# Kernel tuning notes

Measured on AMD Instinct MI355X. Metric: run time of the kernel, lower is better.

The kernel has to match this reference:

```python
import jax, jax.numpy as jnp
import numpy as np

N = 100000
E = 1600000
D_IN, D_HID, D_OUT = 128, 128, 128


def gcn_conv(x, edge_index, W, b):
    """PyG GCNConv with default symmetric normalization and added self-loops.
    out = D^{-1/2} (A + I) D^{-1/2} (x W) + b, edge weights = 1.
    """
    n = x.shape[0]
    h = x @ W                                   # [N, D_out]
    src, dst = edge_index[0], edge_index[1]     # messages flow src -> dst
    ones = jnp.ones(src.shape[0], dtype=x.dtype)
    # degree includes the self-loop (+1), computed on the target index as in PyG
    deg = jax.ops.segment_sum(ones, dst, num_segments=n) + 1.0  # [N]
    dinv = jax.lax.rsqrt(deg)                   # deg >= 1 so safe
    norm = dinv[src] * dinv[dst]                # [E]
    msg = h[src] * norm[:, None]                # [E, D_out]
    agg = jax.ops.segment_sum(msg, dst, num_segments=n)
    # self-loop contribution: norm = dinv_i * dinv_i = 1/deg_i
    out = agg + h * (dinv * dinv)[:, None] + b
    return out


def layer_norm(x, gamma, beta, eps=1e-5):
    mu = jnp.mean(x, axis=-1, keepdims=True)
    var = jnp.mean(jnp.square(x - mu), axis=-1, keepdims=True)
    return (x - mu) * jax.lax.rsqrt(var + eps) * gamma + beta


def setup_inputs() -> dict:
    key = jax.random.key(0)
    ks = jax.random.split(key, 8)
    x = jax.random.normal(ks[0], (N, D_IN), dtype=jnp.float32)
    edge_index = jax.random.randint(ks[1], (2, E), 0, N, dtype=jnp.int64)
    s1 = 1.0 / np.sqrt(D_IN)
    s2 = 1.0 / np.sqrt(D_HID)
    W1 = jax.random.uniform(ks[2], (D_IN, D_HID), jnp.float32, -s1, s1)
    b1 = jnp.zeros((D_HID,), jnp.float32)
    W2 = jax.random.uniform(ks[3], (D_HID, D_OUT), jnp.float32, -s2, s2)
    b2 = jnp.zeros((D_OUT,), jnp.float32)
    gamma = jnp.ones((D_OUT,), jnp.float32)
    beta = jnp.zeros((D_OUT,), jnp.float32)
    return {"x": x, "edge_index": edge_index, "W1": W1, "b1": b1,
            "W2": W2, "b2": b2, "gamma": gamma, "beta": beta}


def reference(x, edge_index, W1, b1, W2, b2, gamma, beta):
    h = gcn_conv(x, edge_index, W1, b1)
    h = jax.nn.relu(h)
    # dropout is identity in eval mode (deterministic reference)
    h = gcn_conv(h, edge_index, W2, b2)
    return layer_norm(h, gamma, beta)
```

## Files before the change

kernel.cpp:

```cpp
#include <hip/hip_runtime.h>


#define N_NODES 100000
#define N_EDGES 1600000
#define NBLK_N  391
#define NB      196
#define BKT_CAP 8960
#define BIN_GRID 391
#define GEMM_GRID 1563

typedef unsigned int  u32;
typedef unsigned short u16;
typedef unsigned char u8;
typedef unsigned long long u64;
typedef __attribute__((ext_vector_type(8))) short bf16x8;
typedef __attribute__((ext_vector_type(4))) float f32x4;

__device__ __forceinline__ float bflo(u32 u){ return __uint_as_float(u << 16); }
__device__ __forceinline__ float bfhi(u32 u){ return __uint_as_float(u & 0xFFFF0000u); }
__device__ __forceinline__ u32 f2b(float f){
  u32 u = __float_as_uint(f);
  return (u + 0x7FFFu + ((u >> 16) & 1u)) >> 16;
}
__device__ __forceinline__ u32 pack2(float a, float b){ return f2b(a) | (f2b(b) << 16); }
__device__ __forceinline__ u32 clampN(int s){
  u32 u = (u32)s;
  return (u < (u32)N_NODES) ? u : (u32)(N_NODES - 1);
}

__global__ __launch_bounds__(64) void detect(const int* __restrict__ ei,
                                             int* __restrict__ flags){
  int l = threadIdx.x;
  int nzodd = (ei[2 * l + 1] != 0) ? 1 : 0;
  #pragma unroll
  for (int o = 32; o > 0; o >>= 1) nzodd += __shfl_xor(nzodd, o, 64);
  if (l == 0) flags[1] = (nzodd == 0) ? 1 : 0;
}


__device__ __forceinline__ void build_wfrag(u16* wfrag, const float* __restrict__ W,
                                            int tid){
  #pragma unroll
  for (int i = 0; i < 8; ++i){
    int fid   = tid + i * 256;
    int lane  = fid & 63;
    int kb    = (fid >> 6) & 3;
    int ntile = fid >> 8;
    int n  = ntile * 16 + (lane & 15);
    int k0 = kb * 32 + (lane >> 4) * 8;
    u16 tmp[8];
    #pragma unroll
    for (int j = 0; j < 8; ++j) tmp[j] = (u16)f2b(W[(k0 + j) * 128 + n]);
    *(bf16x8*)(wfrag + (size_t)fid * 8) = *(const bf16x8*)tmp;
  }
}

__device__ __forceinline__ void gemm_tail(const u16* wfrag, const bf16x8 afrag[4],
                                          int rowbase, int lane,
                                          u16* __restrict__ Hout, int nrows){
  const int m = lane & 15, q = lane >> 4;
  f32x4 acc[8];
  #pragma unroll
  for (int n = 0; n < 8; ++n) acc[n] = (f32x4){0.f, 0.f, 0.f, 0.f};
  #pragma unroll
  for (int n = 0; n < 8; ++n){
    #pragma unroll
    for (int kb = 0; kb < 4; ++kb){
      bf16x8 bfrag = *(const bf16x8*)(wfrag + ((size_t)(n * 4 + kb) * 64 + lane) * 8);
      acc[n] = __builtin_amdgcn_mfma_f32_16x16x32_bf16(afrag[kb], bfrag, acc[n], 0, 0, 0);
    }
  }
  #pragma unroll
  for (int r = 0; r < 4; ++r){
    int orow = rowbase + q * 4 + r;
    if (orow < nrows){
      u16* Or = Hout + (size_t)orow * 128 + m;
      #pragma unroll
      for (int n = 0; n < 8; ++n) Or[n * 16] = (u16)f2b(acc[n][r]);
    }
  }
}

__device__ __forceinline__ void gemm_f32_body(u16* wfrag, const float* __restrict__ A,
                                              const float* __restrict__ W,
                                              u16* __restrict__ Hout, int nrows, int bid){
  build_wfrag(wfrag, W, threadIdx.x);
  __syncthreads();
  const int lane = threadIdx.x & 63;
  const int wv   = threadIdx.x >> 6;
  const int rowbase = bid * 64 + wv * 16;
  const int row  = rowbase + (lane & 15);
  const int rowc = (row < nrows) ? row : (nrows - 1);
  const int q    = lane >> 4;
  bf16x8 afrag[4];
  const float* Ar = A + (size_t)rowc * 128;
  #pragma unroll
  for (int kb = 0; kb < 4; ++kb){
    f32x4 p0 = *(const f32x4*)(Ar + kb * 32 + q * 8);
    f32x4 p1 = *(const f32x4*)(Ar + kb * 32 + q * 8 + 4);
    bf16x8 f;
    f[0] = (short)f2b(p0[0]); f[1] = (short)f2b(p0[1]);
    f[2] = (short)f2b(p0[2]); f[3] = (short)f2b(p0[3]);
    f[4] = (short)f2b(p1[0]); f[5] = (short)f2b(p1[1]);
    f[6] = (short)f2b(p1[2]); f[7] = (short)f2b(p1[3]);
    afrag[kb] = f;
  }
  gemm_tail(wfrag, afrag, rowbase, lane, Hout, nrows);
}

__device__ __forceinline__ void gemm_bf16_body(u16* wfrag, const u16* __restrict__ A,
                                               const float* __restrict__ W,
                                               u16* __restrict__ Hout, int nrows, int bid){
  build_wfrag(wfrag, W, threadIdx.x);
  __syncthreads();
  const int lane = threadIdx.x & 63;
  const int wv   = threadIdx.x >> 6;
  const int rowbase = bid * 64 + wv * 16;
  const int row  = rowbase + (lane & 15);
  const int rowc = (row < nrows) ? row : (nrows - 1);
  const int q    = lane >> 4;
  bf16x8 afrag[4];
  const u16* Ar = A + (size_t)rowc * 128;
  #pragma unroll
  for (int kb = 0; kb < 4; ++kb)
    afrag[kb] = *(const bf16x8*)(Ar + kb * 32 + q * 8);
  gemm_tail(wfrag, afrag, rowbase, lane, Hout, nrows);
}


__device__ __forceinline__ void binA_body(u32* cnt ,
                                          const int* __restrict__ ei,
                                          u32* __restrict__ binned,
                                          u32* __restrict__ bucket_fill, int bb){
  u32* gbase = cnt + 256;
  u32* flagp = cnt + 512;
  const int tid = threadIdx.x;
  cnt[tid] = 0;
  if (tid < 64){
    int nz = (ei[2 * tid + 1] != 0) ? 1 : 0;
    u64 b = __ballot(nz);
    if (tid == 0) *flagp = (b == 0ull) ? 1u : 0u;
  }
  __syncthreads();
  const int i64  = (int)*flagp;
  const int base = bb * 4096;
  u32 pk[16], rk[16], bk[16];
  #pragma unroll
  for (int j = 0; j < 16; ++j){
    int e = base + tid + j * 256;
    bk[j] = 0xFFFFFFFFu;
    if (e < N_EDGES){
      int dsti = i64 ? ei[2 * N_EDGES + 2 * e] : ei[N_EDGES + e];
      int srci = i64 ? ei[2 * e]               : ei[e];
      u32 ud = clampN(dsti), us = clampN(srci);
      u32 b = ud >> 9;
      bk[j] = b;
      pk[j] = us | ((ud & 511u) << 17);
      rk[j] = atomicAdd(&cnt[b], 1u);
    }
  }
  __syncthreads();
  u32 c = cnt[tid];
  u32 old = 0;
  if (c) old = atomicAdd(&bucket_fill[tid < NB ? tid : 0], tid < NB ? c : 0u);
  gbase[tid] = old;
  __syncthreads();
  #pragma unroll
  for (int j = 0; j < 16; ++j){
    if (bk[j] != 0xFFFFFFFFu){
      u32 idx = gbase[bk[j]] + rk[j];
      if (idx < BKT_CAP) binned[(size_t)bk[j] * BKT_CAP + idx] = pk[j];
    }
  }
}


__global__ __launch_bounds__(256) void fused_gemm_bin(const float* __restrict__ A,
                                                      const float* __restrict__ W,
                                                      u16* __restrict__ Hout,
                                                      const int* __restrict__ ei,
                                                      u32* __restrict__ binned,
                                                      u32* __restrict__ bucket_fill){
  __shared__ u16 smem[16384];
  if (blockIdx.x < GEMM_GRID){
    gemm_f32_body(smem, A, W, Hout, N_NODES, blockIdx.x);
  } else {
    binA_body((u32*)smem, ei, binned, bucket_fill, blockIdx.x - GEMM_GRID);
  }
}

__global__ __launch_bounds__(256) void gemm_f32in(const float* __restrict__ A,
                                                  const float* __restrict__ W,
                                                  u16* __restrict__ Hout){
  __shared__ u16 smem[16384];
  gemm_f32_body(smem, A, W, Hout, N_NODES, blockIdx.x);
}
__global__ __launch_bounds__(256) void gemm_bf16in(const u16* __restrict__ A,
                                                   const float* __restrict__ W,
                                                   u16* __restrict__ Hout){
  __shared__ u16 smem[16384];
  gemm_bf16_body(smem, A, W, Hout, N_NODES, blockIdx.x);
}


__global__ __launch_bounds__(256) void fill_sort(const u32* __restrict__ binned,
                                                 const u32* __restrict__ bucket_fill,
                                                 int* __restrict__ offs,
                                                 float* __restrict__ dinv,
                                                 int* __restrict__ srclist){
  __shared__ u32 cnt[512];
  __shared__ u32 sc[512];
  __shared__ u32 red[256];
  const int b   = blockIdx.x;
  const int tid = threadIdx.x;
  cnt[tid] = 0; cnt[tid + 256] = 0;
  __syncthreads();

  u32 n = bucket_fill[b]; if (n > BKT_CAP) n = BKT_CAP;
  const u32* eb = binned + (size_t)b * BKT_CAP;

  for (u32 i = tid; i < n; i += 256)
    atomicAdd(&cnt[eb[i] >> 17], 1u);

  u32 v = 0;
  if (tid < b && tid < NB){
    u32 f = bucket_fill[tid];
    v = (f > BKT_CAP) ? BKT_CAP : f;
  }
  red[tid] = v;
  __syncthreads();
  for (int o = 128; o > 0; o >>= 1){
    if (tid < o) red[tid] += red[tid + o];
    __syncthreads();
  }
  const u32 base = red[0];
  __syncthreads();

  u32 pair = cnt[2 * tid] + cnt[2 * tid + 1];
  red[tid] = pair;
  __syncthreads();
  for (int o = 1; o < 256; o <<= 1){
    u32 add = (tid >= o) ? red[tid - o] : 0;
    __syncthreads();
    red[tid] += add;
    __syncthreads();
  }
  u32 pex = red[tid] - pair;
  sc[2 * tid]     = pex;
  sc[2 * tid + 1] = pex + cnt[2 * tid];
  __syncthreads();

  const u32 basenode = (u32)b << 9;
  #pragma unroll
  for (int h = 0; h < 2; ++h){
    u32 l = tid + h * 256;
    u32 node = basenode + l;
    if (node < (u32)N_NODES){
      offs[node] = (int)(base + sc[l]);
      dinv[node] = rsqrtf((float)cnt[l] + 1.0f);
    }
  }
  if (b == NB - 1 && tid == 0) offs[N_NODES] = (int)(base + n);

  __syncthreads();
  cnt[tid] = 0; cnt[tid + 256] = 0;
  __syncthreads();
  for (u32 i = tid; i < n; i += 256){
    u32 pk = eb[i];
    u32 d  = pk >> 17;
    u32 r  = atomicAdd(&cnt[d], 1u);
    srclist[base + sc[d] + r] = (int)(pk & 0x1FFFFu);
  }
}


__global__ __launch_bounds__(256) void count_deg(const int* __restrict__ ei,
                                                 const int* __restrict__ flags,
                                                 int* __restrict__ deg){
  int e   = blockIdx.x * 256 + threadIdx.x;
  int i64 = flags[1];
  int dst = i64 ? ei[2 * N_EDGES + 2 * e] : ei[N_EDGES + e];
  if ((unsigned)dst < (unsigned)N_NODES) atomicAdd(&deg[dst], 1);
}

__global__ __launch_bounds__(256) void fill_edges(const int* __restrict__ ei,
                                                  const int* __restrict__ flags,
                                                  int* __restrict__ woff,
                                                  int* __restrict__ srclist){
  int e   = blockIdx.x * 256 + threadIdx.x;
  int i64 = flags[1];
  int dst = i64 ? ei[2 * N_EDGES + 2 * e] : ei[N_EDGES + e];
  int src = i64 ? ei[2 * e]               : ei[e];
  if ((unsigned)dst < (unsigned)N_NODES){
    int p = atomicAdd(&woff[dst], 1);
    if ((unsigned)p < (unsigned)N_EDGES) srclist[p] = clampN(src);
  }
}

__global__ __launch_bounds__(256) void scan1(const int* __restrict__ deg,
                                             int* __restrict__ offs,
                                             int* __restrict__ bsum,
                                             float* __restrict__ dinv){
  __shared__ int sh[256];
  int t = threadIdx.x;
  int i = blockIdx.x * 256 + t;
  int v = (i < N_NODES) ? deg[i] : 0;
  if (i < N_NODES) dinv[i] = rsqrtf((float)v + 1.0f);
  sh[t] = v;
  __syncthreads();
  for (int o = 1; o < 256; o <<= 1){
    int add = (t >= o) ? sh[t - o] : 0;
    __syncthreads();
    sh[t] += add;
    __syncthreads();
  }
  if (i < N_NODES) offs[i] = sh[t] - v;
  if (t == 255)    bsum[blockIdx.x] = sh[255];
}

__global__ __launch_bounds__(512) void scan2(const int* __restrict__ bsum,
                                             int* __restrict__ bofs){
  __shared__ int sh[512];
  int t = threadIdx.x;
  int v = (t < NBLK_N) ? bsum[t] : 0;
  sh[t] = v;
  __syncthreads();
  for (int o = 1; o < 512; o <<= 1){
    int add = (t >= o) ? sh[t - o] : 0;
    __syncthreads();
    sh[t] += add;
    __syncthreads();
  }
  if (t < NBLK_N) bofs[t] = sh[t] - v;
}

__global__ __launch_bounds__(256) void finalize_offs(int* __restrict__ offs,
                                                     const int* __restrict__ bofs,
                                                     int* __restrict__ woff){
  int i = blockIdx.x * 256 + threadIdx.x;
  if (i < N_NODES){
    int o = offs[i] + bofs[blockIdx.x];
    offs[i] = o;
    woff[i] = o;
  }
  if (i == 0) offs[N_NODES] = N_EDGES;
}


#define GATHER_EDGE(sv, A0, A1)                         \
  { u32 s_ = (u32)(sv);                                 \
    float w_ = dinv[s_];                                \
    u32 h_ = H[s_ * 64 + lane];                         \
    A0 = fmaf(w_, bflo(h_), A0);                        \
    A1 = fmaf(w_, bfhi(h_), A1); }

__global__ __launch_bounds__(256) void gather_relu(const int* __restrict__ offs,
                                                   const int* __restrict__ srcl,
                                                   const u32* __restrict__ H,
                                                   const float* __restrict__ dinv,
                                                   const float* __restrict__ bias,
                                                   u32* __restrict__ X2){
  const int node = blockIdx.x * 4 + (threadIdx.x >> 6);
  const int lane = threadIdx.x & 63;
  int beg = offs[node], end = offs[node + 1];
  if (end > N_EDGES) end = N_EDGES;
  if (beg < 0 || beg > end) beg = end;
  float a0 = 0.f, a1 = 0.f, c0 = 0.f, c1 = 0.f;
  int e = beg;
  for (; e + 8 <= end; e += 8){
    int s0=srcl[e],s1=srcl[e+1],s2=srcl[e+2],s3=srcl[e+3];
    int s4=srcl[e+4],s5=srcl[e+5],s6=srcl[e+6],s7=srcl[e+7];
    GATHER_EDGE(s0,a0,a1) GATHER_EDGE(s1,c0,c1)
    GATHER_EDGE(s2,a0,a1) GATHER_EDGE(s3,c0,c1)
    GATHER_EDGE(s4,a0,a1) GATHER_EDGE(s5,c0,c1)
    GATHER_EDGE(s6,a0,a1) GATHER_EDGE(s7,c0,c1)
  }
  for (; e + 4 <= end; e += 4){
    int s0=srcl[e],s1=srcl[e+1],s2=srcl[e+2],s3=srcl[e+3];
    GATHER_EDGE(s0,a0,a1) GATHER_EDGE(s1,c0,c1)
    GATHER_EDGE(s2,a0,a1) GATHER_EDGE(s3,c0,c1)
  }
  for (; e < end; ++e){ int s0=srcl[e]; GATHER_EDGE(s0,a0,a1) }
  a0 += c0;  a1 += c1;
  float di = dinv[node];
  u32 hs = H[(u32)node * 64 + lane];
  float b0 = bias[2 * lane], b1v = bias[2 * lane + 1];
  float v0 = fmaf(a0, di, fmaf(bflo(hs), di * di, b0));
  float v1 = fmaf(a1, di, fmaf(bfhi(hs), di * di, b1v));
  X2[(u32)node * 64 + lane] = pack2(fmaxf(v0, 0.f), fmaxf(v1, 0.f));
}

__global__ __launch_bounds__(256) void gather_ln(const int* __restrict__ offs,
                                                 const int* __restrict__ srcl,
                                                 const u32* __restrict__ H,
                                                 const float* __restrict__ dinv,
                                                 const float* __restrict__ bias,
                                                 const float* __restrict__ gamma,
                                                 const float* __restrict__ beta,
                                                 float* __restrict__ out){
  const int node = blockIdx.x * 4 + (threadIdx.x >> 6);
  const int lane = threadIdx.x & 63;
  int beg = offs[node], end = offs[node + 1];
  if (end > N_EDGES) end = N_EDGES;
  if (beg < 0 || beg > end) beg = end;
  float a0 = 0.f, a1 = 0.f, c0 = 0.f, c1 = 0.f;
  int e = beg;
  for (; e + 8 <= end; e += 8){
    int s0=srcl[e],s1=srcl[e+1],s2=srcl[e+2],s3=srcl[e+3];
    int s4=srcl[e+4],s5=srcl[e+5],s6=srcl[e+6],s7=srcl[e+7];
    GATHER_EDGE(s0,a0,a1) GATHER_EDGE(s1,c0,c1)
    GATHER_EDGE(s2,a0,a1) GATHER_EDGE(s3,c0,c1)
    GATHER_EDGE(s4,a0,a1) GATHER_EDGE(s5,c0,c1)
    GATHER_EDGE(s6,a0,a1) GATHER_EDGE(s7,c0,c1)
  }
  for (; e + 4 <= end; e += 4){
    int s0=srcl[e],s1=srcl[e+1],s2=srcl[e+2],s3=srcl[e+3];
    GATHER_EDGE(s0,a0,a1) GATHER_EDGE(s1,c0,c1)
    GATHER_EDGE(s2,a0,a1) GATHER_EDGE(s3,c0,c1)
  }
  for (; e < end; ++e){ int s0=srcl[e]; GATHER_EDGE(s0,a0,a1) }
  a0 += c0;  a1 += c1;
  float di = dinv[node];
  u32 hs = H[(u32)node * 64 + lane];
  float b0 = bias[2 * lane], b1v = bias[2 * lane + 1];
  float v0 = fmaf(a0, di, fmaf(bflo(hs), di * di, b0));
  float v1 = fmaf(a1, di, fmaf(bfhi(hs), di * di, b1v));

  float s2 = v0 + v1;
  #pragma unroll
  for (int o = 32; o > 0; o >>= 1) s2 += __shfl_xor(s2, o, 64);
  float mu = s2 * 0.0078125f;
  float d0 = v0 - mu, d1 = v1 - mu;
  float qq = d0 * d0 + d1 * d1;
  #pragma unroll
  for (int o = 32; o > 0; o >>= 1) qq += __shfl_xor(qq, o, 64);
  float rr = rsqrtf(qq * 0.0078125f + 1e-5f);

  float g0 = gamma[2 * lane], g1 = gamma[2 * lane + 1];
  float t0 = beta[2 * lane],  t1 = beta[2 * lane + 1];
  *(float2*)(out + (size_t)node * 128 + 2 * lane) =
      make_float2(fmaf(d0 * rr, g0, t0), fmaf(d1 * rr, g1, t1));
}


extern "C" void kernel_launch(void* const* d_in, const int* in_sizes, int n_in,
                              void* d_out, int out_size, void* d_ws, size_t ws_size,
                              hipStream_t stream){
  const float* x  = (const float*)d_in[0];
  const int*   ei = (const int*)d_in[1];
  const float* W1 = (const float*)d_in[2];
  const float* b1 = (const float*)d_in[3];
  const float* W2 = (const float*)d_in[4];
  const float* b2 = (const float*)d_in[5];
  const float* gm = (const float*)d_in[6];
  const float* bt = (const float*)d_in[7];

  char* ws = (char*)d_ws;
  size_t off = 0;
  auto carve = [&](size_t bytes) -> void* {
    void* p = ws + off;
    off = (off + bytes + 255) & ~(size_t)255;
    return p;
  };
  int*   flags       = (int*)  carve(64);
  u32*   bucket_fill = (u32*)  carve(NB * 4);
  int*   offs        = (int*)  carve((size_t)(N_NODES + 1) * 4);
  float* dinv        = (float*)carve((size_t)N_NODES * 4);
  int*   srclist     = (int*)  carve((size_t)N_EDGES * 4);
  int*   deg         = (int*)  carve((size_t)N_NODES * 4);
  int*   bsum        = (int*)  carve(2048);
  int*   bofs        = (int*)  carve(2048);

  size_t bin_bytes = (size_t)NB * BKT_CAP * 4;
  u32* binned = (u32*)carve(bin_bytes);
  bool use_binned = (ws_size >= off);
  if (!use_binned) off = (size_t)((char*)binned - ws);

  size_t h_bytes = (size_t)N_NODES * 128 * 2;
  u32* H1 = (u32*)d_out;
  u32* X2 = (u32*)d_out + 6400000;
  u32* H2 = (ws_size >= off + h_bytes) ? (u32*)carve(h_bytes) : (u32*)d_in[0];

  if (use_binned){
    hipMemsetAsync(bucket_fill, 0, NB * 4, stream);
    fused_gemm_bin<<<GEMM_GRID + BIN_GRID, 256, 0, stream>>>(x, W1, (u16*)H1, ei,
                                                             binned, bucket_fill);
    fill_sort     <<<NB, 256, 0, stream>>>(binned, bucket_fill, offs, dinv, srclist);
  } else {
    hipMemsetAsync(deg, 0, (size_t)N_NODES * 4, stream);
    detect        <<<1,             64,  0, stream>>>(ei, flags);
    count_deg     <<<N_EDGES / 256, 256, 0, stream>>>(ei, flags, deg);
    scan1         <<<NBLK_N,        256, 0, stream>>>(deg, offs, bsum, dinv);
    scan2         <<<1,             512, 0, stream>>>(bsum, bofs);
    finalize_offs <<<NBLK_N,        256, 0, stream>>>(offs, bofs, deg );
    fill_edges    <<<N_EDGES / 256, 256, 0, stream>>>(ei, flags, deg , srclist);
    gemm_f32in    <<<GEMM_GRID,     256, 0, stream>>>(x, W1, (u16*)H1);
  }

  gather_relu <<<N_NODES / 4, 256, 0, stream>>>(offs, srclist, H1, dinv, b1, X2);
  gemm_bf16in <<<GEMM_GRID,   256, 0, stream>>>((const u16*)X2, W2, (u16*)H2);
  gather_ln   <<<N_NODES / 4, 256, 0, stream>>>(offs, srclist, H2, dinv, b2, gm, bt,
                                                (float*)d_out);
}
```

Before: 311.6 us.

## Split gather_relu feature dim into halves and process edge pairs per wave

```diff
diff --git a/kernel.cpp b/kernel.cpp
--- a/kernel.cpp
+++ b/kernel.cpp
@@ -8,6 +8,7 @@
 #define BKT_CAP 8960
 #define BIN_GRID 391
 #define GEMM_GRID 1563
+#define RELU_GRID 50000
 
 typedef unsigned int  u32;
 typedef unsigned short u16;
@@ -347,48 +348,70 @@
 }
 
 
+
+#define GATHER_PAIR(e_, A0, A1)                         \
+  { int s0_ = srcl[e_], s1_ = srcl[(e_) + 1];           \
+    u32 sv_ = (u32)(sub ? s1_ : s0_);                   \
+    float w_ = dinv[sv_];                               \
+    u32 h_ = H[sv_ * 64 + hb + cl];                     \
+    A0 = fmaf(w_, bflo(h_), A0);                        \
+    A1 = fmaf(w_, bfhi(h_), A1); }
+
+__global__ __launch_bounds__(256) void gather_relu(const int* __restrict__ offs,
+                                                   const int* __restrict__ srcl,
+                                                   const u32* __restrict__ H,
+                                                   const float* __restrict__ dinv,
+                                                   const float* __restrict__ bias,
+                                                   u32* __restrict__ X2){
+  const int b  = blockIdx.x;
+  const int g  = b >> 3, r = b & 7;
+  const int h  = r >> 2;
+  const int q  = r & 3;
+  const int wv = threadIdx.x >> 6;
+  const int node = g * 16 + q * 4 + wv;
+  const int lane = threadIdx.x & 63;
+  const int sub  = lane >> 5;
+  const int cl   = lane & 31;
+  const int hb   = h * 32;
+
+  int beg = offs[node], end = offs[node + 1];
+  if (end > N_EDGES) end = N_EDGES;
+  if (beg < 0 || beg > end) beg = end;
+  float a0 = 0.f, a1 = 0.f, c0 = 0.f, c1 = 0.f;
+  int e = beg;
+  for (; e + 8 <= end; e += 8){
+    GATHER_PAIR(e,     a0, a1) GATHER_PAIR(e + 2, c0, c1)
+    GATHER_PAIR(e + 4, a0, a1) GATHER_PAIR(e + 6, c0, c1)
+  }
+  for (; e + 2 <= end; e += 2){ GATHER_PAIR(e, a0, a1) }
+  if (e < end){
+    int s0_ = srcl[e];
+    u32 sv_ = (u32)s0_;
+    float w_ = sub ? 0.0f : dinv[sv_];
+    u32 h_ = H[sv_ * 64 + hb + cl];
+    a0 = fmaf(w_, bflo(h_), a0);
+    a1 = fmaf(w_, bfhi(h_), a1);
+  }
+  a0 += c0;  a1 += c1;
+  a0 += __shfl_xor(a0, 32, 64);
+  a1 += __shfl_xor(a1, 32, 64);
+
+  float di = dinv[node];
+  u32 hs = H[(u32)node * 64 + hb + cl];
+  float b0 = bias[h * 64 + 2 * cl], b1v = bias[h * 64 + 2 * cl + 1];
+  float v0 = fmaf(a0, di, fmaf(bflo(hs), di * di, b0));
+  float v1 = fmaf(a1, di, fmaf(bfhi(hs), di * di, b1v));
+  if (sub == 0)
+    X2[(u32)node * 64 + hb + cl] = pack2(fmaxf(v0, 0.f), fmaxf(v1, 0.f));
+}
+
+
 #define GATHER_EDGE(sv, A0, A1)                         \
   { u32 s_ = (u32)(sv);                                 \
     float w_ = dinv[s_];                                \
     u32 h_ = H[s_ * 64 + lane];                         \
     A0 = fmaf(w_, bflo(h_), A0);                        \
     A1 = fmaf(w_, bfhi(h_), A1); }
-
-__global__ __launch_bounds__(256) void gather_relu(const int* __restrict__ offs,
-                                                   const int* __restrict__ srcl,
-                                                   const u32* __restrict__ H,
-                                                   const float* __restrict__ dinv,
-                                                   const float* __restrict__ bias,
-                                                   u32* __restrict__ X2){
-  const int node = blockIdx.x * 4 + (threadIdx.x >> 6);
-  const int lane = threadIdx.x & 63;
-  int beg = offs[node], end = offs[node + 1];
-  if (end > N_EDGES) end = N_EDGES;
-  if (beg < 0 || beg > end) beg = end;
-  float a0 = 0.f, a1 = 0.f, c0 = 0.f, c1 = 0.f;
-  int e = beg;
-  for (; e + 8 <= end; e += 8){
-    int s0=srcl[e],s1=srcl[e+1],s2=srcl[e+2],s3=srcl[e+3];
-    int s4=srcl[e+4],s5=srcl[e+5],s6=srcl[e+6],s7=srcl[e+7];
-    GATHER_EDGE(s0,a0,a1) GATHER_EDGE(s1,c0,c1)
-    GATHER_EDGE(s2,a0,a1) GATHER_EDGE(s3,c0,c1)
-    GATHER_EDGE(s4,a0,a1) GATHER_EDGE(s5,c0,c1)
-    GATHER_EDGE(s6,a0,a1) GATHER_EDGE(s7,c0,c1)
-  }
-  for (; e + 4 <= end; e += 4){
-    int s0=srcl[e],s1=srcl[e+1],s2=srcl[e+2],s3=srcl[e+3];
-    GATHER_EDGE(s0,a0,a1) GATHER_EDGE(s1,c0,c1)
-    GATHER_EDGE(s2,a0,a1) GATHER_EDGE(s3,c0,c1)
-  }
-  for (; e < end; ++e){ int s0=srcl[e]; GATHER_EDGE(s0,a0,a1) }
-  a0 += c0;  a1 += c1;
-  float di = dinv[node];
-  u32 hs = H[(u32)node * 64 + lane];
-  float b0 = bias[2 * lane], b1v = bias[2 * lane + 1];
-  float v0 = fmaf(a0, di, fmaf(bflo(hs), di * di, b0));
-  float v1 = fmaf(a1, di, fmaf(bfhi(hs), di * di, b1v));
-  X2[(u32)node * 64 + lane] = pack2(fmaxf(v0, 0.f), fmaxf(v1, 0.f));
-}
 
 __global__ __launch_bounds__(256) void gather_ln(const int* __restrict__ offs,
                                                  const int* __restrict__ srcl,
@@ -497,7 +520,7 @@
     gemm_f32in    <<<GEMM_GRID,     256, 0, stream>>>(x, W1, (u16*)H1);
   }
 
-  gather_relu <<<N_NODES / 4, 256, 0, stream>>>(offs, srclist, H1, dinv, b1, X2);
+  gather_relu <<<RELU_GRID,   256, 0, stream>>>(offs, srclist, H1, dinv, b1, X2);
   gemm_bf16in <<<GEMM_GRID,   256, 0, stream>>>((const u16*)X2, W2, (u16*)H2);
   gather_ln   <<<N_NODES / 4, 256, 0, stream>>>(offs, srclist, H2, dinv, b2, gm, bt,
                                                 (float*)d_out);
```

Result: slower. 351.9 us (+12.9%).

## Fuse layer-1 gather+ReLU with layer-2 GEMM via shared-memory tile

Applied to the files above, without the earlier changes.

```diff
diff --git a/kernel.cpp b/kernel.cpp
--- a/kernel.cpp
+++ b/kernel.cpp
@@ -8,6 +8,7 @@
 #define BKT_CAP 8960
 #define BIN_GRID 391
 #define GEMM_GRID 1563
+#define MM_GRID  6250
 
 typedef unsigned int  u32;
 typedef unsigned short u16;
@@ -105,25 +106,6 @@
     f[6] = (short)f2b(p1[2]); f[7] = (short)f2b(p1[3]);
     afrag[kb] = f;
   }
-  gemm_tail(wfrag, afrag, rowbase, lane, Hout, nrows);
-}
-
-__device__ __forceinline__ void gemm_bf16_body(u16* wfrag, const u16* __restrict__ A,
-                                               const float* __restrict__ W,
-                                               u16* __restrict__ Hout, int nrows, int bid){
-  build_wfrag(wfrag, W, threadIdx.x);
-  __syncthreads();
-  const int lane = threadIdx.x & 63;
-  const int wv   = threadIdx.x >> 6;
-  const int rowbase = bid * 64 + wv * 16;
-  const int row  = rowbase + (lane & 15);
-  const int rowc = (row < nrows) ? row : (nrows - 1);
-  const int q    = lane >> 4;
-  bf16x8 afrag[4];
-  const u16* Ar = A + (size_t)rowc * 128;
-  #pragma unroll
-  for (int kb = 0; kb < 4; ++kb)
-    afrag[kb] = *(const bf16x8*)(Ar + kb * 32 + q * 8);
   gemm_tail(wfrag, afrag, rowbase, lane, Hout, nrows);
 }
 
@@ -195,12 +177,6 @@
   __shared__ u16 smem[16384];
   gemm_f32_body(smem, A, W, Hout, N_NODES, blockIdx.x);
 }
-__global__ __launch_bounds__(256) void gemm_bf16in(const u16* __restrict__ A,
-                                                   const float* __restrict__ W,
-                                                   u16* __restrict__ Hout){
-  __shared__ u16 smem[16384];
-  gemm_bf16_body(smem, A, W, Hout, N_NODES, blockIdx.x);
-}
 
 
 __global__ __launch_bounds__(256) void fill_sort(const u32* __restrict__ binned,
@@ -354,41 +330,99 @@
     A0 = fmaf(w_, bflo(h_), A0);                        \
     A1 = fmaf(w_, bfhi(h_), A1); }
 
-__global__ __launch_bounds__(256) void gather_relu(const int* __restrict__ offs,
-                                                   const int* __restrict__ srcl,
-                                                   const u32* __restrict__ H,
-                                                   const float* __restrict__ dinv,
-                                                   const float* __restrict__ bias,
-                                                   u32* __restrict__ X2){
-  const int node = blockIdx.x * 4 + (threadIdx.x >> 6);
+#define GATHER_BODY                                     \
+  int beg = offs[node], end = offs[node + 1];           \
+  if (end > N_EDGES) end = N_EDGES;                     \
+  if (beg < 0 || beg > end) beg = end;                  \
+  float a0 = 0.f, a1 = 0.f, c0 = 0.f, c1 = 0.f;         \
+  int e = beg;                                          \
+  for (; e + 8 <= end; e += 8){                         \
+    int s0=srcl[e],s1=srcl[e+1],s2=srcl[e+2],s3=srcl[e+3]; \
+    int s4=srcl[e+4],s5=srcl[e+5],s6=srcl[e+6],s7=srcl[e+7]; \
+    GATHER_EDGE(s0,a0,a1) GATHER_EDGE(s1,c0,c1)         \
+    GATHER_EDGE(s2,a0,a1) GATHER_EDGE(s3,c0,c1)         \
+    GATHER_EDGE(s4,a0,a1) GATHER_EDGE(s5,c0,c1)         \
+    GATHER_EDGE(s6,a0,a1) GATHER_EDGE(s7,c0,c1)         \
+  }                                                     \
+  for (; e + 4 <= end; e += 4){                         \
+    int s0=srcl[e],s1=srcl[e+1],s2=srcl[e+2],s3=srcl[e+3]; \
+    GATHER_EDGE(s0,a0,a1) GATHER_EDGE(s1,c0,c1)         \
+    GATHER_EDGE(s2,a0,a1) GATHER_EDGE(s3,c0,c1)         \
+  }                                                     \
+  for (; e < end; ++e){ int s0=srcl[e]; GATHER_EDGE(s0,a0,a1) } \
+  a0 += c0;  a1 += c1;                                  \
+  float di = dinv[node];                                \
+  u32 hs = H[(u32)node * 64 + lane];                    \
+  float v0 = fmaf(a0, di, fmaf(bflo(hs), di * di, bb0)); \
+  float v1 = fmaf(a1, di, fmaf(bfhi(hs), di * di, bb1));
+
+
+__global__ __launch_bounds__(256) void gather_relu_mm(const int* __restrict__ offs,
+                                                      const int* __restrict__ srcl,
+                                                      const u32* __restrict__ H,
+                                                      const float* __restrict__ dinv,
+                                                      const float* __restrict__ bias,
+                                                      const float* __restrict__ W2,
+                                                      u16* __restrict__ H2){
+  __shared__ u16 atile[16 * 136];
+  const int wv   = threadIdx.x >> 6;
   const int lane = threadIdx.x & 63;
-  int beg = offs[node], end = offs[node + 1];
-  if (end > N_EDGES) end = N_EDGES;
-  if (beg < 0 || beg > end) beg = end;
-  float a0 = 0.f, a1 = 0.f, c0 = 0.f, c1 = 0.f;
-  int e = beg;
-  for (; e + 8 <= end; e += 8){
-    int s0=srcl[e],s1=srcl[e+1],s2=srcl[e+2],s3=srcl[e+3];
-    int s4=srcl[e+4],s5=srcl[e+5],s6=srcl[e+6],s7=srcl[e+7];
-    GATHER_EDGE(s0,a0,a1) GATHER_EDGE(s1,c0,c1)
-    GATHER_EDGE(s2,a0,a1) GATHER_EDGE(s3,c0,c1)
-    GATHER_EDGE(s4,a0,a1) GATHER_EDGE(s5,c0,c1)
-    GATHER_EDGE(s6,a0,a1) GATHER_EDGE(s7,c0,c1)
-  }
-  for (; e + 4 <= end; e += 4){
-    int s0=srcl[e],s1=srcl[e+1],s2=srcl[e+2],s3=srcl[e+3];
-    GATHER_EDGE(s0,a0,a1) GATHER_EDGE(s1,c0,c1)
-    GATHER_EDGE(s2,a0,a1) GATHER_EDGE(s3,c0,c1)
-  }
-  for (; e < end; ++e){ int s0=srcl[e]; GATHER_EDGE(s0,a0,a1) }
-  a0 += c0;  a1 += c1;
-  float di = dinv[node];
-  u32 hs = H[(u32)node * 64 + lane];
-  float b0 = bias[2 * lane], b1v = bias[2 * lane + 1];
-  float v0 = fmaf(a0, di, fmaf(bflo(hs), di * di, b0));
-  float v1 = fmaf(a1, di, fmaf(bfhi(hs), di * di, b1v));
-  X2[(u32)node * 64 + lane] = pack2(fmaxf(v0, 0.f), fmaxf(v1, 0.f));
-}
+  const int m = lane & 15, q = lane >> 4;
+  const int nodebase = blockIdx.x * 16;
+
+  bf16x8 bfragR[2][4];
+  {
+    const int nn = (wv * 2) * 16 + m;
+    const int k0 = q * 8;
+    #pragma unroll
+    for (int t = 0; t < 2; ++t){
+      #pragma unroll
+      for (int kb = 0; kb < 4; ++kb){
+        bf16x8 f;
+        #pragma unroll
+        for (int j = 0; j < 8; ++j)
+          f[j] = (short)f2b(W2[(kb * 32 + k0 + j) * 128 + nn + t * 16]);
+        bfragR[t][kb] = f;
+      }
+    }
+  }
+
+  const float bb0 = bias[2 * lane], bb1 = bias[2 * lane + 1];
+
+  #pragma unroll 1
+  for (int j4 = 0; j4 < 4; ++j4){
+    const int node = nodebase + wv * 4 + j4;
+    GATHER_BODY
+    *(u32*)(atile + (size_t)(wv * 4 + j4) * 136 + 2 * lane) =
+        pack2(fmaxf(v0, 0.f), fmaxf(v1, 0.f));
+  }
+  __syncthreads();
+
+  bf16x8 afrag[4];
+  #pragma unroll
+  for (int kb = 0; kb < 4; ++kb)
+    afrag[kb] = *(const bf16x8*)(atile + (size_t)m * 136 + kb * 32 + q * 8);
+  f32x4 acc[2];
+  acc[0] = (f32x4){0.f, 0.f, 0.f, 0.f};
+  acc[1] = (f32x4){0.f, 0.f, 0.f, 0.f};
+  #pragma unroll
+  for (int t = 0; t < 2; ++t){
+    #pragma unroll
+    for (int kb = 0; kb < 4; ++kb)
+      acc[t] = __builtin_amdgcn_mfma_f32_16x16x32_bf16(afrag[kb], bfragR[t][kb],
+                                                       acc[t], 0, 0, 0);
+  }
+  #pragma unroll
+  for (int t = 0; t < 2; ++t){
+    const int col = (wv * 2 + t) * 16 + m;
+    #pragma unroll
+    for (int rr = 0; rr < 4; ++rr){
+      const int row = q * 4 + rr;
+      H2[(size_t)(nodebase + row) * 128 + col] = (u16)f2b(acc[t][rr]);
+    }
+  }
+}
+
 
 __global__ __launch_bounds__(256) void gather_ln(const int* __restrict__ offs,
                                                  const int* __restrict__ srcl,
@@ -400,31 +434,8 @@
                                                  float* __restrict__ out){
   const int node = blockIdx.x * 4 + (threadIdx.x >> 6);
   const int lane = threadIdx.x & 63;
-  int beg = offs[node], end = offs[node + 1];
-  if (end > N_EDGES) end = N_EDGES;
-  if (beg < 0 || beg > end) beg = end;
-  float a0 = 0.f, a1 = 0.f, c0 = 0.f, c1 = 0.f;
-  int e = beg;
-  for (; e + 8 <= end; e += 8){
-    int s0=srcl[e],s1=srcl[e+1],s2=srcl[e+2],s3=srcl[e+3];
-    int s4=srcl[e+4],s5=srcl[e+5],s6=srcl[e+6],s7=srcl[e+7];
-    GATHER_EDGE(s0,a0,a1) GATHER_EDGE(s1,c0,c1)
-    GATHER_EDGE(s2,a0,a1) GATHER_EDGE(s3,c0,c1)
-    GATHER_EDGE(s4,a0,a1) GATHER_EDGE(s5,c0,c1)
-    GATHER_EDGE(s6,a0,a1) GATHER_EDGE(s7,c0,c1)
-  }
-  for (; e + 4 <= end; e += 4){
-    int s0=srcl[e],s1=srcl[e+1],s2=srcl[e+2],s3=srcl[e+3];
-    GATHER_EDGE(s0,a0,a1) GATHER_EDGE(s1,c0,c1)
-    GATHER_EDGE(s2,a0,a1) GATHER_EDGE(s3,c0,c1)
-  }
-  for (; e < end; ++e){ int s0=srcl[e]; GATHER_EDGE(s0,a0,a1) }
-  a0 += c0;  a1 += c1;
-  float di = dinv[node];
-  u32 hs = H[(u32)node * 64 + lane];
-  float b0 = bias[2 * lane], b1v = bias[2 * lane + 1];
-  float v0 = fmaf(a0, di, fmaf(bflo(hs), di * di, b0));
-  float v1 = fmaf(a1, di, fmaf(bfhi(hs), di * di, b1v));
+  const float bb0 = bias[2 * lane], bb1 = bias[2 * lane + 1];
+  GATHER_BODY
 
   float s2 = v0 + v1;
   #pragma unroll
@@ -478,7 +489,6 @@
 
   size_t h_bytes = (size_t)N_NODES * 128 * 2;
   u32* H1 = (u32*)d_out;
-  u32* X2 = (u32*)d_out + 6400000;
   u32* H2 = (ws_size >= off + h_bytes) ? (u32*)carve(h_bytes) : (u32*)d_in[0];
 
   if (use_binned){
@@ -497,8 +507,8 @@
     gemm_f32in    <<<GEMM_GRID,     256, 0, stream>>>(x, W1, (u16*)H1);
   }
 
-  gather_relu <<<N_NODES / 4, 256, 0, stream>>>(offs, srclist, H1, dinv, b1, X2);
-  gemm_bf16in <<<GEMM_GRID,   256, 0, stream>>>((const u16*)X2, W2, (u16*)H2);
-  gather_ln   <<<N_NODES / 4, 256, 0, stream>>>(offs, srclist, H2, dinv, b2, gm, bt,
-                                                (float*)d_out);
-}
+  gather_relu_mm <<<MM_GRID,     256, 0, stream>>>(offs, srclist, H1, dinv, b1, W2,
+                                                   (u16*)H2);
+  gather_ln      <<<N_NODES / 4, 256, 0, stream>>>(offs, srclist, H2, dinv, b2, gm, bt,
+                                                   (float*)d_out);
+}
```

Result: slower. 350.4 us (+12.5%).
